# Kernel tuning notes

Hardware: AMD Instinct MI355X
Metric: run time of the kernel (lower is better)

Reference implementation:

```python
import jax, jax.numpy as jnp
import numpy as np

N = 50000
IN_DIM = 128
HIDDEN = 64
OUT_DIM = 10
HEADS = 4
NUM_LAYERS = 3
NEG_SLOPE = 0.2


def _glorot(key, shape):
    fan_in, fan_out = shape[0], shape[-1]
    lim = jnp.sqrt(6.0 / (fan_in + fan_out))
    return jax.random.uniform(key, shape, jnp.float32, -lim, lim)


def setup_inputs() -> dict:
    key = jax.random.key(0)
    ks = jax.random.split(key, 2 + 4 * NUM_LAYERS + 2)
    inp = {}
    inp["x"] = jax.random.normal(ks[0], (N, IN_DIM), jnp.float32)
    inp["edge_index"] = jax.random.randint(ks[1], (2, 800000), 0, N, jnp.int64)
    ki = 2
    for i in range(NUM_LAYERS):
        d_in = IN_DIM if i == 0 else HIDDEN
        inp[f"W{i}"] = _glorot(ks[ki], (d_in, HEADS * HIDDEN)); ki += 1
        inp[f"asrc{i}"] = _glorot(ks[ki], (HEADS, HIDDEN)); ki += 1
        inp[f"adst{i}"] = _glorot(ks[ki], (HEADS, HIDDEN)); ki += 1
        inp[f"b{i}"] = jnp.zeros((HIDDEN,), jnp.float32); ki += 1
    inp["fcW"] = _glorot(ks[ki], (HIDDEN, OUT_DIM)); ki += 1
    inp["fcb"] = jnp.zeros((OUT_DIM,), jnp.float32)
    return inp


def _gat_layer(x, W, a_src, a_dst, bias, src, dst):
    # x: [N, d_in] -> h: [N, H, D]
    h = (x @ W).reshape(N, HEADS, HIDDEN)
    al_s = jnp.einsum("nhd,hd->nh", h, a_src)  # [N, H]
    al_d = jnp.einsum("nhd,hd->nh", h, a_dst)  # [N, H]
    e = jax.nn.leaky_relu(al_s[src] + al_d[dst], NEG_SLOPE)  # [E, H]
    # segment softmax over incoming edges of each destination node
    m = jax.ops.segment_max(e, dst, num_segments=N)  # [N, H]
    ex = jnp.exp(e - m[dst])
    denom = jax.ops.segment_sum(ex, dst, num_segments=N)  # [N, H]
    alpha = ex / denom[dst]  # [E, H]
    # weighted scatter-add aggregation: [E,H,D] -> [N,H,D]
    out = jax.ops.segment_sum(alpha[:, :, None] * h[src], dst, num_segments=N)
    return out.mean(axis=1) + bias  # concat=False -> head mean, [N, HIDDEN]


def reference(x, edge_index, W0, asrc0, adst0, b0, W1, asrc1, adst1, b1,
              W2, asrc2, adst2, b2, fcW, fcb):
    # PyG GATConv default: add self-loops
    loops = jnp.arange(N, dtype=edge_index.dtype)
    src = jnp.concatenate([edge_index[0], loops])
    dst = jnp.concatenate([edge_index[1], loops])
    params = [(W0, asrc0, adst0, b0), (W1, asrc1, adst1, b1), (W2, asrc2, adst2, b2)]
    h = x
    for (W, a_s, a_d, b) in params:
        h = _gat_layer(h, W, a_s, a_d, b, src, dst)
        h = jax.nn.elu(h)
        # dropout p=0.3 is a no-op in eval mode
    return h @ fcW + fcb  # [N, OUT_DIM]
```

## Files before the change

### kernel.cpp

```cpp
#include <hip/hip_runtime.h>
#include <hip/hip_fp16.h>
#include <math.h>

#define N_NODES 50000
#define IN_DIM  128
#define HIDDEN  64
#define OUT_DIM 10
#define HEADS   4
#define E_RAW   800000
#define E_TOT   (E_RAW + N_NODES)
#define NEG_SLOPE 0.2f

#define NB_SCAN 196
#define NB_GEMH 782
#define NB_NODE 12500
#define NB_FILL 831

#define PAD 64

typedef _Float16 half8 __attribute__((ext_vector_type(8)));
typedef float floatx4 __attribute__((ext_vector_type(4)));

__global__ void prep_kernel(const int* __restrict__ ei, int* __restrict__ cnt,
                            int* __restrict__ flag,
                            const float* __restrict__ X, __half* __restrict__ Xh,
                            const float* __restrict__ W0, const float* __restrict__ W1,
                            const float* __restrict__ W2,
                            __half* __restrict__ Wtf0, __half* __restrict__ Wtf1,
                            __half* __restrict__ Wtf2,
                            const float* __restrict__ as0, const float* __restrict__ ad0,
                            const float* __restrict__ as1, const float* __restrict__ ad1,
                            const float* __restrict__ as2, const float* __restrict__ ad2,
                            float* __restrict__ Wa0, float* __restrict__ Wa1,
                            float* __restrict__ Wa2) {
    int bid = blockIdx.x, t = threadIdx.x;
    if (bid < 196) {
        int i = bid * 256 + t;
        if (i < N_NODES) {
            cnt[i] = 0;
            const float4* X4 = (const float4*)(X + (size_t)i * 128);
            __half2* xh2 = (__half2*)(Xh + (size_t)i * 128);
#pragma unroll 8
            for (int k4 = 0; k4 < 32; k4++) {
                float4 v = X4[k4];
                xh2[k4 * 2]     = __float22half2_rn(make_float2(v.x, v.y));
                xh2[k4 * 2 + 1] = __float22half2_rn(make_float2(v.z, v.w));
            }
        }
    } else if (bid == 196) {
        __shared__ int anyv;
        if (t == 0) anyv = 0;
        __syncthreads();
        int idx = 2 * (t * 3100 + 17) + 1;
        if (ei[idx] != 0) atomicOr(&anyv, 1);
        __syncthreads();
        if (t == 0) flag[0] = anyv;
    } else if (bid < 229) {
        int i = (bid - 197) * 256 + t;
        int KC, DIN, f;
        const float* W; __half* Wtf;
        if (i < 4096)      { f = i;        KC = 16; DIN = 128; W = W0; Wtf = Wtf0; }
        else if (i < 6144) { f = i - 4096; KC = 8;  DIN = 64;  W = W1; Wtf = Wtf1; }
        else if (i < 8192) { f = i - 6144; KC = 8;  DIN = 64;  W = W2; Wtf = Wtf2; }
        else return;
        int lane = f & 63, kc = (f >> 6) % KC, ct = f / (64 * KC);
        int m = lane & 15, quad = lane >> 4;
        int col = ct * 16 + m;
        __half tmp[8];
#pragma unroll
        for (int j = 0; j < 8; j++) {
            int k = kc * 32 + quad * 8 + j;
            int h = k / DIN, kk = k % DIN;
            tmp[j] = __float2half(0.25f * W[kk * 256 + h * 64 + col]);
        }
        *(uint4*)(Wtf + (size_t)f * 8) = *(uint4*)tmp;
    } else {
        int b = bid - 229;
        int l, k;
        if (b < 128)      { l = 0; k = b; }
        else if (b < 192) { l = 1; k = b - 128; }
        else              { l = 2; k = b - 192; }
        const float* W  = (l == 0) ? W0 : (l == 1) ? W1 : W2;
        const float* as = (l == 0) ? as0 : (l == 1) ? as1 : as2;
        const float* ad = (l == 0) ? ad0 : (l == 1) ? ad1 : ad2;
        float* Wa       = (l == 0) ? Wa0 : (l == 1) ? Wa1 : Wa2;
        int h = t >> 6, d = t & 63;
        float wv = W[k * 256 + h * 64 + d];
        float ss = wv * as[h * 64 + d];
        float dd = wv * ad[h * 64 + d];
#pragma unroll
        for (int o = 1; o < 64; o <<= 1) {
            ss += __shfl_xor(ss, o, 64);
            dd += __shfl_xor(dd, o, 64);
        }
        if (d == 0) {
            Wa[k * 8 + h]     = ss;
            Wa[k * 8 + 4 + h] = dd;
        }
    }
}


__device__ __forceinline__ void al128_body(
    int n, const float* __restrict__ X, const float* __restrict__ Wa,
    float* __restrict__ AL) {
    if (n >= N_NODES) return;
    const float4* X4 = (const float4*)(X + (size_t)n * 128);
    float s[8];
#pragma unroll
    for (int j = 0; j < 8; j++) s[j] = 0.f;
#pragma unroll 4
    for (int k4 = 0; k4 < 32; k4++) {
        float4 v = X4[k4];
#pragma unroll
        for (int j = 0; j < 8; j++)
            s[j] += v.x * Wa[(k4 * 4 + 0) * 8 + j] + v.y * Wa[(k4 * 4 + 1) * 8 + j]
                  + v.z * Wa[(k4 * 4 + 2) * 8 + j] + v.w * Wa[(k4 * 4 + 3) * 8 + j];
    }
    *(float4*)(AL + n * 8)     = make_float4(s[0], s[1], s[2], s[3]);
    *(float4*)(AL + n * 8 + 4) = make_float4(s[4], s[5], s[6], s[7]);
}

__device__ __forceinline__ void al64_body(
    int n, const float* __restrict__ X, const float* __restrict__ Wa,
    float* __restrict__ AL) {
    if (n >= N_NODES) return;
    const float4* X4 = (const float4*)(X + (size_t)n * 64);
    float s[8];
#pragma unroll
    for (int j = 0; j < 8; j++) s[j] = 0.f;
#pragma unroll 4
    for (int k4 = 0; k4 < 16; k4++) {
        float4 v = X4[k4];
#pragma unroll
        for (int j = 0; j < 8; j++)
            s[j] += v.x * Wa[(k4 * 4 + 0) * 8 + j] + v.y * Wa[(k4 * 4 + 1) * 8 + j]
                  + v.z * Wa[(k4 * 4 + 2) * 8 + j] + v.w * Wa[(k4 * 4 + 3) * 8 + j];
    }
    *(float4*)(AL + n * 8)     = make_float4(s[0], s[1], s[2], s[3]);
    *(float4*)(AL + n * 8 + 4) = make_float4(s[4], s[5], s[6], s[7]);
}

__global__ void __launch_bounds__(256) fill_al(
    const int* __restrict__ ei, int* __restrict__ cnt,
    int* __restrict__ esrc_pad, const int* __restrict__ flag,
    const float* __restrict__ X, const float* __restrict__ Wa0,
    float* __restrict__ AL) {
    if (blockIdx.x < NB_FILL) {
        int base = blockIdx.x * 1024 + threadIdx.x;
        int sh = flag[0] ? 0 : 1;
        int srcs[4], dsts[4], poss[4];
        bool valid[4];
#pragma unroll
        for (int j = 0; j < 4; j++) {
            int t = base + j * 256;
            valid[j] = (t < E_TOT);
            srcs[j] = 0; dsts[j] = 0;
            if (valid[j]) {
                if (t < E_RAW) { srcs[j] = ei[t << sh]; dsts[j] = ei[(E_RAW + t) << sh]; }
                else           { srcs[j] = t - E_RAW;   dsts[j] = srcs[j]; }
            }
        }
#pragma unroll
        for (int j = 0; j < 4; j++)
            if (valid[j]) poss[j] = atomicAdd(&cnt[dsts[j]], 1);
#pragma unroll
        for (int j = 0; j < 4; j++)
            if (valid[j] && poss[j] < PAD)
                esrc_pad[(dsts[j] << 6) + poss[j]] = srcs[j];
    } else {
        int n = (blockIdx.x - NB_FILL) * 256 + threadIdx.x;
        al128_body(n, X, Wa0, AL);
    }
}

template <int DIN>
__global__ void __launch_bounds__(256) agg_x(
    const __half* __restrict__ X16, const float* __restrict__ AL,
    const int* __restrict__ cnt, const int* __restrict__ esrc,
    __half* __restrict__ AGG) {
    int wave = threadIdx.x >> 6, lane = threadIdx.x & 63;
    int n = blockIdx.x * 4 + wave;

    int start = n << 6;
    int c = cnt[n]; if (c > PAD) c = PAD;
    const float4* AL4 = (const float4*)AL;

    float4 ad = AL4[n * 2 + 1];
    int my_s = 0;
    float4 myE = make_float4(0.f, 0.f, 0.f, 0.f);
    if (lane < c) {
        my_s = esrc[start + lane];
        float4 as = AL4[my_s * 2];
        float v0 = as.x + ad.x; v0 = fmaxf(v0, NEG_SLOPE * v0);
        float v1 = as.y + ad.y; v1 = fmaxf(v1, NEG_SLOPE * v1);
        float v2 = as.z + ad.z; v2 = fmaxf(v2, NEG_SLOPE * v2);
        float v3 = as.w + ad.w; v3 = fmaxf(v3, NEG_SLOPE * v3);
        myE = make_float4(__expf(v0), __expf(v1), __expf(v2), __expf(v3));
    }

    float acc0[4] = {0.f, 0.f, 0.f, 0.f};
    float acc1[4] = {0.f, 0.f, 0.f, 0.f};
    float d0 = 0.f, d1 = 0.f, d2 = 0.f, d3 = 0.f;

#define BCAST_E(idx) make_float4(__shfl(myE.x, (idx), 64), __shfl(myE.y, (idx), 64), \
                                 __shfl(myE.z, (idx), 64), __shfl(myE.w, (idx), 64))
#define EDGE_BODY(E, xlo, xhi)                                      \
    {                                                               \
        d0 += E.x; d1 += E.y; d2 += E.z; d3 += E.w;                 \
        acc0[0] += E.x * xlo; acc0[1] += E.y * xlo;                 \
        acc0[2] += E.z * xlo; acc0[3] += E.w * xlo;                 \
        if (DIN == 128) {                                           \
            acc1[0] += E.x * xhi; acc1[1] += E.y * xhi;             \
            acc1[2] += E.z * xhi; acc1[3] += E.w * xhi;             \
        }                                                           \
    }

    for (int base = 0; base < c; base += 4) {
        int m = c - base;
        int r1 = (1 < m ? 1 : 0), r2 = (2 < m ? 2 : 0), r3 = (3 < m ? 3 : 0);
        int s0 = __shfl(my_s, base, 64);
        int s1 = __shfl(my_s, base + r1, 64);
        int s2 = __shfl(my_s, base + r2, 64);
        int s3 = __shfl(my_s, base + r3, 64);
        float4 E0 = BCAST_E(base);
        float4 E1 = BCAST_E(base + r1);
        float4 E2 = BCAST_E(base + r2);
        float4 E3 = BCAST_E(base + r3);
        float x0lo, x0hi = 0.f, x1lo, x1hi = 0.f, x2lo, x2hi = 0.f, x3lo, x3hi = 0.f;
        if (DIN == 128) {
            float2 v0 = __half22float2(*(const __half2*)(X16 + (size_t)s0 * 128 + 2 * lane));
            float2 v1 = __half22float2(*(const __half2*)(X16 + (size_t)s1 * 128 + 2 * lane));
            float2 v2 = __half22float2(*(const __half2*)(X16 + (size_t)s2 * 128 + 2 * lane));
            float2 v3 = __half22float2(*(const __half2*)(X16 + (size_t)s3 * 128 + 2 * lane));
            x0lo = v0.x; x0hi = v0.y; x1lo = v1.x; x1hi = v1.y;
            x2lo = v2.x; x2hi = v2.y; x3lo = v3.x; x3hi = v3.y;
        } else {
            x0lo = __half2float(X16[(size_t)s0 * 64 + lane]);
            x1lo = __half2float(X16[(size_t)s1 * 64 + lane]);
            x2lo = __half2float(X16[(size_t)s2 * 64 + lane]);
            x3lo = __half2float(X16[(size_t)s3 * 64 + lane]);
        }
        EDGE_BODY(E0, x0lo, x0hi);
        if (m > 1) EDGE_BODY(E1, x1lo, x1hi);
        if (m > 2) EDGE_BODY(E2, x2lo, x2hi);
        if (m > 3) EDGE_BODY(E3, x3lo, x3hi);
    }
#undef EDGE_BODY
#undef BCAST_E

    float dn[4] = {d0, d1, d2, d3};
    if (DIN == 128) {
#pragma unroll
        for (int h = 0; h < 4; h++) {
            float inv = 1.f / dn[h];
            *(__half2*)(AGG + (size_t)n * 512 + h * 128 + 2 * lane) =
                __float22half2_rn(make_float2(acc0[h] * inv, acc1[h] * inv));
        }
    } else {
#pragma unroll
        for (int h = 0; h < 4; h++)
            AGG[(size_t)n * 256 + h * 64 + lane] = __float2half(acc0[h] / dn[h]);
    }
}

template <int K>
__global__ void __launch_bounds__(256) gemm_out(
    const __half* __restrict__ AGG, const __half* __restrict__ Wtf,
    const float* __restrict__ bias, float* __restrict__ XOUT,
    __half* __restrict__ X16) {
    __shared__ _Float16 lds[16384];
    const int KC = K / 32;
    const int NCHUNK = (K == 512) ? 2 : 1;
    const int CTC = 4 / NCHUNK;
    int t = threadIdx.x;
    int w = t >> 6, lane = t & 63;
    int m = lane & 15, quad = lane >> 4;
    int n0 = blockIdx.x * 64;
    int nr = n0 + w * 16 + m;
    int nc = (nr < N_NODES) ? nr : (N_NODES - 1);

    half8 afrag[KC];
#pragma unroll
    for (int kc = 0; kc < KC; kc++)
        afrag[kc] = *(const half8*)(AGG + (size_t)nc * K + kc * 32 + quad * 8);

    floatx4 accs[4];
    const uint4* Wg = (const uint4*)Wtf;
#pragma unroll
    for (int c = 0; c < NCHUNK; c++) {
        __syncthreads();
        uint4* dstl = (uint4*)lds;
        const uint4* srcg = Wg + (size_t)c * 2048;
#pragma unroll
        for (int q = 0; q < 8; q++) dstl[t + 256 * q] = srcg[t + 256 * q];
        __syncthreads();
#pragma unroll
        for (int ctl = 0; ctl < CTC; ctl++) {
            floatx4 acc = {0.f, 0.f, 0.f, 0.f};
#pragma unroll
            for (int kc = 0; kc < KC; kc++) {
                half8 b = *(const half8*)&lds[((ctl * KC + kc) * 64 + lane) * 8];
                acc = __builtin_amdgcn_mfma_f32_16x16x32_f16(afrag[kc], b, acc, 0, 0, 0);
            }
            accs[c * CTC + ctl] = acc;
        }
    }
    int nodeBase = n0 + w * 16 + quad * 4;
#pragma unroll
    for (int ct = 0; ct < 4; ct++) {
        int col = ct * 16 + m;
        float bv = bias[col];
#pragma unroll
        for (int i = 0; i < 4; i++) {
            int node = nodeBase + i;
            if (node < N_NODES) {
                float v = accs[ct][i] + bv;
                v = v > 0.f ? v : (__expf(v) - 1.f);
                XOUT[(size_t)node * 64 + col] = v;
                if (X16) X16[(size_t)node * 64 + col] = __float2half(v);
            }
        }
    }
}

__global__ void __launch_bounds__(256) al64_kernel(
    const float* __restrict__ X, const float* __restrict__ Wa,
    float* __restrict__ AL) {
    int n = blockIdx.x * 256 + threadIdx.x;
    al64_body(n, X, Wa, AL);
}

__global__ void __launch_bounds__(256) fc_kernel(
    const float* __restrict__ X, const float* __restrict__ fcW,
    const float* __restrict__ fcb, float* __restrict__ OUT) {
    __shared__ float ws[64 * 10];
    __shared__ float bs[10];
    int t = threadIdx.x;
    for (int i = t; i < 640; i += 256) ws[i] = fcW[i];
    if (t < 10) bs[t] = fcb[t];
    __syncthreads();
    int n = blockIdx.x * 256 + t;
    if (n >= N_NODES) return;
    float acc[10];
#pragma unroll
    for (int c = 0; c < 10; c++) acc[c] = bs[c];
    for (int d = 0; d < 64; d++) {
        float x = X[n * 64 + d];
#pragma unroll
        for (int c = 0; c < 10; c++) acc[c] += x * ws[d * 10 + c];
    }
#pragma unroll
    for (int c = 0; c < 10; c++) OUT[n * 10 + c] = acc[c];
}

extern "C" void kernel_launch(void* const* d_in, const int* in_sizes, int n_in,
                              void* d_out, int out_size, void* d_ws, size_t ws_size,
                              hipStream_t stream) {
    const float* x     = (const float*)d_in[0];
    const int*   ei    = (const int*)d_in[1];
    const float* W[3]    = {(const float*)d_in[2], (const float*)d_in[6], (const float*)d_in[10]};
    const float* asrc[3] = {(const float*)d_in[3], (const float*)d_in[7], (const float*)d_in[11]};
    const float* adst[3] = {(const float*)d_in[4], (const float*)d_in[8], (const float*)d_in[12]};
    const float* bias[3] = {(const float*)d_in[5], (const float*)d_in[9], (const float*)d_in[13]};
    const float* fcW = (const float*)d_in[14];
    const float* fcb = (const float*)d_in[15];
    float* out = (float*)d_out;

    char* ws = (char*)d_ws;
    size_t off = 0;
    auto alloc = [&](size_t bytes) {
        void* p = ws + off;
        off = (off + bytes + 255) & ~(size_t)255;
        return p;
    };
    __half* AGG     = (__half*)alloc((size_t)N_NODES * 512 * 2);
    float*  AL      = (float*)alloc((size_t)N_NODES * 8 * 4);
    float*  XA      = (float*)alloc((size_t)N_NODES * 64 * 4);
    __half* Xh0     = (__half*)alloc((size_t)N_NODES * 128 * 2);
    __half* X16     = (__half*)alloc((size_t)N_NODES * 64 * 2);
    __half* Wtf0    = (__half*)alloc(4096 * 8 * 2);
    __half* Wtf1    = (__half*)alloc(2048 * 8 * 2);
    __half* Wtf2    = (__half*)alloc(2048 * 8 * 2);
    float*  Wa0     = (float*)alloc(128 * 8 * 4);
    float*  Wa1     = (float*)alloc(64 * 8 * 4);
    float*  Wa2     = (float*)alloc(64 * 8 * 4);
    int* cnt      = (int*)alloc((size_t)N_NODES * 4);
    int* esrc_pad = (int*)alloc((size_t)N_NODES * PAD * 4);
    int* flag     = (int*)alloc(256 * 4);

    prep_kernel<<<485, 256, 0, stream>>>(ei, cnt, flag, x, Xh0,
                                         W[0], W[1], W[2],
                                         Wtf0, Wtf1, Wtf2,
                                         asrc[0], adst[0], asrc[1], adst[1],
                                         asrc[2], adst[2], Wa0, Wa1, Wa2);
    fill_al<<<NB_FILL + NB_SCAN, 256, 0, stream>>>(ei, cnt, esrc_pad, flag,
                                                   x, Wa0, AL);
    agg_x<128><<<NB_NODE, 256, 0, stream>>>(Xh0, AL, cnt, esrc_pad, AGG);
    gemm_out<512><<<NB_GEMH, 256, 0, stream>>>(AGG, Wtf0, bias[0], XA, X16);
    al64_kernel<<<NB_SCAN, 256, 0, stream>>>(XA, Wa1, AL);
    agg_x<64><<<NB_NODE, 256, 0, stream>>>(X16, AL, cnt, esrc_pad, AGG);
    gemm_out<256><<<NB_GEMH, 256, 0, stream>>>(AGG, Wtf1, bias[1], XA, X16);
    al64_kernel<<<NB_SCAN, 256, 0, stream>>>(XA, Wa2, AL);
    agg_x<64><<<NB_NODE, 256, 0, stream>>>(X16, AL, cnt, esrc_pad, AGG);
    gemm_out<256><<<NB_GEMH, 256, 0, stream>>>(AGG, Wtf2, bias[2], XA, nullptr);

    fc_kernel<<<NB_SCAN, 256, 0, stream>>>(XA, fcW, fcb, out);
}
```

Before: 377.9 us.

## Fuse attention-logit projection into GEMM epilogue and batch 8 gathers via LDS

The per-layer al64_kernel is folded into the gemm_out epilogue. The epilogue computes the source and destination attention logits from the ELU output in registers, using shuffle reductions across the 16 column lanes, so the fp32 XA write and re-read are skipped for layers 0 and 1. The aggregation kernel now stages edge weights and source indices in LDS and issues 8 independent row gathers per iteration instead of 4 shuffle-broadcast loads, which raises memory-level parallelism. The costs are extra epilogue ALU and shuffle work in the GEMM. The gather loop also reads padded LDS entries (zero weight, source 0) past the edge count.

```diff
diff --git a/kernel.cpp b/kernel.cpp
--- a/kernel.cpp
+++ b/kernel.cpp
@@ -121,26 +121,6 @@
     *(float4*)(AL + n * 8 + 4) = make_float4(s[4], s[5], s[6], s[7]);
 }
 
-__device__ __forceinline__ void al64_body(
-    int n, const float* __restrict__ X, const float* __restrict__ Wa,
-    float* __restrict__ AL) {
-    if (n >= N_NODES) return;
-    const float4* X4 = (const float4*)(X + (size_t)n * 64);
-    float s[8];
-#pragma unroll
-    for (int j = 0; j < 8; j++) s[j] = 0.f;
-#pragma unroll 4
-    for (int k4 = 0; k4 < 16; k4++) {
-        float4 v = X4[k4];
-#pragma unroll
-        for (int j = 0; j < 8; j++)
-            s[j] += v.x * Wa[(k4 * 4 + 0) * 8 + j] + v.y * Wa[(k4 * 4 + 1) * 8 + j]
-                  + v.z * Wa[(k4 * 4 + 2) * 8 + j] + v.w * Wa[(k4 * 4 + 3) * 8 + j];
-    }
-    *(float4*)(AL + n * 8)     = make_float4(s[0], s[1], s[2], s[3]);
-    *(float4*)(AL + n * 8 + 4) = make_float4(s[4], s[5], s[6], s[7]);
-}
-
 __global__ void __launch_bounds__(256) fill_al(
     const int* __restrict__ ei, int* __restrict__ cnt,
     int* __restrict__ esrc_pad, const int* __restrict__ flag,
@@ -179,6 +159,8 @@
     const __half* __restrict__ X16, const float* __restrict__ AL,
     const int* __restrict__ cnt, const int* __restrict__ esrc,
     __half* __restrict__ AGG) {
+    __shared__ float ldsE[4][64][4];
+    __shared__ int   ldsS[4][64];
     int wave = threadIdx.x >> 6, lane = threadIdx.x & 63;
     int n = blockIdx.x * 4 + wave;
 
@@ -198,58 +180,45 @@
         float v3 = as.w + ad.w; v3 = fmaxf(v3, NEG_SLOPE * v3);
         myE = make_float4(__expf(v0), __expf(v1), __expf(v2), __expf(v3));
     }
+    *(float4*)&ldsE[wave][lane][0] = myE;
+    ldsS[wave][lane] = my_s;
 
     float acc0[4] = {0.f, 0.f, 0.f, 0.f};
     float acc1[4] = {0.f, 0.f, 0.f, 0.f};
-    float d0 = 0.f, d1 = 0.f, d2 = 0.f, d3 = 0.f;
-
-#define BCAST_E(idx) make_float4(__shfl(myE.x, (idx), 64), __shfl(myE.y, (idx), 64), \
-                                 __shfl(myE.z, (idx), 64), __shfl(myE.w, (idx), 64))
-#define EDGE_BODY(E, xlo, xhi)                                      \
-    {                                                               \
-        d0 += E.x; d1 += E.y; d2 += E.z; d3 += E.w;                 \
-        acc0[0] += E.x * xlo; acc0[1] += E.y * xlo;                 \
-        acc0[2] += E.z * xlo; acc0[3] += E.w * xlo;                 \
-        if (DIN == 128) {                                           \
-            acc1[0] += E.x * xhi; acc1[1] += E.y * xhi;             \
-            acc1[2] += E.z * xhi; acc1[3] += E.w * xhi;             \
-        }                                                           \
-    }
-
-    for (int base = 0; base < c; base += 4) {
-        int m = c - base;
-        int r1 = (1 < m ? 1 : 0), r2 = (2 < m ? 2 : 0), r3 = (3 < m ? 3 : 0);
-        int s0 = __shfl(my_s, base, 64);
-        int s1 = __shfl(my_s, base + r1, 64);
-        int s2 = __shfl(my_s, base + r2, 64);
-        int s3 = __shfl(my_s, base + r3, 64);
-        float4 E0 = BCAST_E(base);
-        float4 E1 = BCAST_E(base + r1);
-        float4 E2 = BCAST_E(base + r2);
-        float4 E3 = BCAST_E(base + r3);
-        float x0lo, x0hi = 0.f, x1lo, x1hi = 0.f, x2lo, x2hi = 0.f, x3lo, x3hi = 0.f;
+    float dn[4]   = {0.f, 0.f, 0.f, 0.f};
+
+    int nIter = (c + 7) >> 3;
+    for (int it = 0; it < nIter; ++it) {
+        int j0 = it << 3;
+        int sv[8];
+#pragma unroll
+        for (int k = 0; k < 8; k++) sv[k] = ldsS[wave][j0 + k];
+        float2 xv2[8]; float xv1[8];
         if (DIN == 128) {
-            float2 v0 = __half22float2(*(const __half2*)(X16 + (size_t)s0 * 128 + 2 * lane));
-            float2 v1 = __half22float2(*(const __half2*)(X16 + (size_t)s1 * 128 + 2 * lane));
-            float2 v2 = __half22float2(*(const __half2*)(X16 + (size_t)s2 * 128 + 2 * lane));
-            float2 v3 = __half22float2(*(const __half2*)(X16 + (size_t)s3 * 128 + 2 * lane));
-            x0lo = v0.x; x0hi = v0.y; x1lo = v1.x; x1hi = v1.y;
-            x2lo = v2.x; x2hi = v2.y; x3lo = v3.x; x3hi = v3.y;
+#pragma unroll
+            for (int k = 0; k < 8; k++)
+                xv2[k] = __half22float2(*(const __half2*)(X16 + (size_t)sv[k] * 128 + 2 * lane));
         } else {
-            x0lo = __half2float(X16[(size_t)s0 * 64 + lane]);
-            x1lo = __half2float(X16[(size_t)s1 * 64 + lane]);
-            x2lo = __half2float(X16[(size_t)s2 * 64 + lane]);
-            x3lo = __half2float(X16[(size_t)s3 * 64 + lane]);
-        }
-        EDGE_BODY(E0, x0lo, x0hi);
-        if (m > 1) EDGE_BODY(E1, x1lo, x1hi);
-        if (m > 2) EDGE_BODY(E2, x2lo, x2hi);
-        if (m > 3) EDGE_BODY(E3, x3lo, x3hi);
-    }
-#undef EDGE_BODY
-#undef BCAST_E
-
-    float dn[4] = {d0, d1, d2, d3};
+#pragma unroll
+            for (int k = 0; k < 8; k++)
+                xv1[k] = __half2float(X16[(size_t)sv[k] * 64 + lane]);
+        }
+#pragma unroll
+        for (int k = 0; k < 8; k++) {
+            float4 E = *(const float4*)&ldsE[wave][j0 + k][0];
+            dn[0] += E.x; dn[1] += E.y; dn[2] += E.z; dn[3] += E.w;
+            if (DIN == 128) {
+                acc0[0] += E.x * xv2[k].x; acc0[1] += E.y * xv2[k].x;
+                acc0[2] += E.z * xv2[k].x; acc0[3] += E.w * xv2[k].x;
+                acc1[0] += E.x * xv2[k].y; acc1[1] += E.y * xv2[k].y;
+                acc1[2] += E.z * xv2[k].y; acc1[3] += E.w * xv2[k].y;
+            } else {
+                acc0[0] += E.x * xv1[k]; acc0[1] += E.y * xv1[k];
+                acc0[2] += E.z * xv1[k]; acc0[3] += E.w * xv1[k];
+            }
+        }
+    }
+
     if (DIN == 128) {
 #pragma unroll
         for (int h = 0; h < 4; h++) {
@@ -267,8 +236,9 @@
 template <int K>
 __global__ void __launch_bounds__(256) gemm_out(
     const __half* __restrict__ AGG, const __half* __restrict__ Wtf,
-    const float* __restrict__ bias, float* __restrict__ XOUT,
-    __half* __restrict__ X16) {
+    const float* __restrict__ bias, const float* __restrict__ Wa,
+    float* __restrict__ XOUT, __half* __restrict__ X16,
+    float* __restrict__ ALout) {
     __shared__ _Float16 lds[16384];
     const int KC = K / 32;
     const int NCHUNK = (K == 512) ? 2 : 1;
@@ -306,29 +276,55 @@
             accs[c * CTC + ctl] = acc;
         }
     }
+    float vv[4][4];
+#pragma unroll
+    for (int ct = 0; ct < 4; ct++) {
+        float bv = bias[ct * 16 + m];
+#pragma unroll
+        for (int i = 0; i < 4; i++) {
+            float v = accs[ct][i] + bv;
+            vv[ct][i] = v > 0.f ? v : (__expf(v) - 1.f);
+        }
+    }
     int nodeBase = n0 + w * 16 + quad * 4;
 #pragma unroll
     for (int ct = 0; ct < 4; ct++) {
         int col = ct * 16 + m;
-        float bv = bias[col];
 #pragma unroll
         for (int i = 0; i < 4; i++) {
             int node = nodeBase + i;
             if (node < N_NODES) {
-                float v = accs[ct][i] + bv;
-                v = v > 0.f ? v : (__expf(v) - 1.f);
-                XOUT[(size_t)node * 64 + col] = v;
-                if (X16) X16[(size_t)node * 64 + col] = __float2half(v);
-            }
-        }
-    }
-}
-
-__global__ void __launch_bounds__(256) al64_kernel(
-    const float* __restrict__ X, const float* __restrict__ Wa,
-    float* __restrict__ AL) {
-    int n = blockIdx.x * 256 + threadIdx.x;
-    al64_body(n, X, Wa, AL);
+                if (XOUT) XOUT[(size_t)node * 64 + col] = vv[ct][i];
+                if (X16)  X16[(size_t)node * 64 + col] = __float2half(vv[ct][i]);
+            }
+        }
+    }
+    if (ALout) {
+        float war[4][8];
+#pragma unroll
+        for (int ct = 0; ct < 4; ct++) {
+            const float4* wp = (const float4*)(Wa + (ct * 16 + m) * 8);
+            float4 a = wp[0], b = wp[1];
+            war[ct][0] = a.x; war[ct][1] = a.y; war[ct][2] = a.z; war[ct][3] = a.w;
+            war[ct][4] = b.x; war[ct][5] = b.y; war[ct][6] = b.z; war[ct][7] = b.w;
+        }
+#pragma unroll
+        for (int i = 0; i < 4; i++) {
+            int node = nodeBase + i;
+            float alm = 0.f;
+#pragma unroll
+            for (int j = 0; j < 8; j++) {
+                float s = vv[0][i] * war[0][j] + vv[1][i] * war[1][j]
+                        + vv[2][i] * war[2][j] + vv[3][i] * war[3][j];
+                s += __shfl_xor(s, 1, 64);
+                s += __shfl_xor(s, 2, 64);
+                s += __shfl_xor(s, 4, 64);
+                s += __shfl_xor(s, 8, 64);
+                if (j == (m & 7)) alm = s;
+            }
+            if (m < 8 && node < N_NODES) ALout[(size_t)node * 8 + m] = alm;
+        }
+    }
 }
 
 __global__ void __launch_bounds__(256) fc_kernel(
@@ -397,13 +393,14 @@
     fill_al<<<NB_FILL + NB_SCAN, 256, 0, stream>>>(ei, cnt, esrc_pad, flag,
                                                    x, Wa0, AL);
     agg_x<128><<<NB_NODE, 256, 0, stream>>>(Xh0, AL, cnt, esrc_pad, AGG);
-    gemm_out<512><<<NB_GEMH, 256, 0, stream>>>(AGG, Wtf0, bias[0], XA, X16);
-    al64_kernel<<<NB_SCAN, 256, 0, stream>>>(XA, Wa1, AL);
+    gemm_out<512><<<NB_GEMH, 256, 0, stream>>>(AGG, Wtf0, bias[0], Wa1,
+                                               nullptr, X16, AL);
     agg_x<64><<<NB_NODE, 256, 0, stream>>>(X16, AL, cnt, esrc_pad, AGG);
-    gemm_out<256><<<NB_GEMH, 256, 0, stream>>>(AGG, Wtf1, bias[1], XA, X16);
-    al64_kernel<<<NB_SCAN, 256, 0, stream>>>(XA, Wa2, AL);
+    gemm_out<256><<<NB_GEMH, 256, 0, stream>>>(AGG, Wtf1, bias[1], Wa2,
+                                               nullptr, X16, AL);
     agg_x<64><<<NB_NODE, 256, 0, stream>>>(X16, AL, cnt, esrc_pad, AGG);
-    gemm_out<256><<<NB_GEMH, 256, 0, stream>>>(AGG, Wtf2, bias[2], XA, nullptr);
+    gemm_out<256><<<NB_GEMH, 256, 0, stream>>>(AGG, Wtf2, bias[2], nullptr,
+                                               XA, nullptr, nullptr);
 
     fc_kernel<<<NB_SCAN, 256, 0, stream>>>(XA, fcW, fcb, out);
 }
```

After: 317.1 us. 1.19x faster.
